# Optimization experiments

Hardware: AMD Instinct MI355X
Metric: run time of the kernel (lower is better)

The kernel has to match this reference:

```python
import jax, jax.numpy as jnp
import numpy as np

FT = 0.2  # clip floor (init arg ft)

def _norm_mat(m):
    # matrix / (count of nonzeros along last dim + 1e-30)
    deg = jnp.sum(m != 0, axis=-1, keepdims=True).astype(m.dtype)
    return m / (deg + 1e-30)

def _l2n(x):
    return x / (jnp.linalg.norm(x, axis=-1, keepdims=True) + 1e-30)

def setup_inputs():
    B, L, D, H, O = 2, 2048, 64, 64, 128
    N = 2 * L
    ks = jax.random.split(jax.random.key(0), 30)
    u = lambda i, s: jax.random.uniform(ks[i], s, jnp.float32)
    g = lambda i, s: jax.random.normal(ks[i], s, jnp.float32) * 0.05
    inp = {}
    inp['word_outputs_0'] = g(0, (B, L, D))
    inp['word_outputs_1'] = g(1, (B, L, D))
    inp['node_hidden'] = g(2, (B, D))
    inp['op_embedding'] = g(3, (B, O, D))
    inp['word_exist_sequence'] = (u(4, (B, N)) < 0.8).astype(jnp.float32)
    inp['word_exist_matrix'] = (u(5, (B, N, N)) < 0.8).astype(jnp.float32)
    inp['word_operator'] = (u(6, (B, N, O)) < 0.02).astype(jnp.float32)
    inp['word_word'] = (u(7, (B, N, N)) < 0.01).astype(jnp.float32)
    inp['depend_0'] = (u(8, (B, L, L)) < 0.05).astype(jnp.float32)
    inp['depend_1'] = (u(9, (B, L, L)) < 0.05).astype(jnp.float32)
    inp['goal_word'] = u(10, (B, N))
    names = [('Wg', (D, H)), ('bg', (H,)), ('Wwk', (D, H)), ('bwk', (H,)),
             ('Wws', (D, H)), ('bws', (H,)), ('Wo', (D, D)), ('bo', (D,)),
             ('Wupd', (3 * H, D)), ('bupd', (D,)), ('Wf', (3 * H + D, D)), ('bf', (D,)),
             ('Wf2', (2 * D, D)), ('bf2', (D,)), ('Wout', (D, D)), ('bout', (D,))]
    for i, (nm, s) in enumerate(names):
        inp[nm] = g(11 + i, s)
    return inp

def _forward(w0, w1, nh, opE, wes, wem, wop, ww, d0, d1, gw,
             Wg, bg, Wwk, bwk, Wws, bws, Wo, bo, Wupd, bupd, Wf, bf, Wf2, bf2, Wout, bout):
    all_w = jnp.concatenate([w0, w1], axis=1)                      # [B,N,D]
    goal_trans = (nh @ Wg + bg)[:, None, :]                        # [B,1,H] (broadcast = expand)
    word_g = _l2n(goal_trans * gw[..., None])                      # [B,N,H]
    word_w_k = _l2n(jnp.matmul(_norm_mat(ww * wem), all_w @ Wwk + bwk))
    ws0 = jnp.matmul(_norm_mat(d0), w0 @ Wws + bws)
    ws1 = jnp.matmul(_norm_mat(d1), w1 @ Wws + bws)
    word_w_s = _l2n(jnp.concatenate([ws0, ws1], axis=1))           # [B,N,H]
    neigh = jnp.concatenate([word_g, word_w_k, word_w_s], axis=-1)  # [B,N,3H]
    forget = jax.nn.sigmoid(jnp.concatenate([all_w, word_g, word_w_k, word_w_s], axis=-1) @ Wf + bf)
    word_updated = jnp.maximum(forget, FT) * all_w + (1.0 - forget) * jax.nn.relu(neigh @ Wupd + bupd)
    adj_op = _norm_mat(jnp.swapaxes(wes[..., None] * wop, 1, 2))   # [B,O,N]
    word_op = jnp.matmul(adj_op, word_updated @ Wo + bo)           # [B,O,D]
    forget2 = jax.nn.sigmoid(jnp.concatenate([opE, word_op], axis=-1) @ Wf2 + bf2)
    op_out = jnp.maximum(forget2, FT) * opE + (1.0 - forget2) * jax.nn.relu(word_op @ Wout + bout)
    # original returns (split(word_updated), op_embedding); concat along node axis here
    return jnp.concatenate([word_updated, op_out], axis=1)         # [B,N+O,D]

def reference(word_outputs_0, word_outputs_1, node_hidden, op_embedding,
              word_exist_sequence, word_exist_matrix, word_operator, word_word,
              depend_0, depend_1, goal_word,
              Wg, bg, Wwk, bwk, Wws, bws, Wo, bo, Wupd, bupd, Wf, bf, Wf2, bf2, Wout, bout):
    return _forward(word_outputs_0, word_outputs_1, node_hidden, op_embedding,
                    word_exist_sequence, word_exist_matrix, word_operator, word_word,
                    depend_0, depend_1, goal_word,
                    Wg, bg, Wwk, bwk, Wws, bws, Wo, bo, Wupd, bupd, Wf, bf, Wf2, bf2, Wout, bout)
```

## Files before the change

### kernel.cpp

```cpp
#include <hip/hip_runtime.h>
#include <cstdint>

typedef unsigned short u16;
typedef unsigned long long u64;

__device__ __forceinline__ u16 f2b(float f){
  union { float f; uint32_t i; } v; v.f = f;
  uint32_t r = v.i + 0x7FFFu + ((v.i >> 16) & 1u);
  return (u16)(r >> 16);
}
__device__ __forceinline__ float b2f(u16 u){
  union { uint32_t i; float f; } v; v.i = ((uint32_t)u) << 16; return v.f;
}
__device__ __forceinline__ float sigmoidf(float x){ return 1.0f / (1.0f + __expf(-x)); }

__device__ __forceinline__ void gl_lds4(const void* g, void* l){
  __builtin_amdgcn_global_load_lds((const __attribute__((address_space(1))) void*)g,
                                   (__attribute__((address_space(3))) void*)l, 4, 0, 0);
}
#define WAIT_VM0() __builtin_amdgcn_s_waitcnt(0x0F70)

__global__ __launch_bounds__(256) void k_bits_all(
    const float* __restrict__ ww, const float* __restrict__ wem,
    const float* __restrict__ d0, const float* __restrict__ d1,
    const float* __restrict__ wes, const float* __restrict__ wop,
    const float* __restrict__ w0, const float* __restrict__ w1,
    const float* __restrict__ nh, const float* __restrict__ Wg, const float* __restrict__ bg,
    const float* __restrict__ Wf, const float* __restrict__ Wupd, const float* __restrict__ Wo,
    u16* __restrict__ psumB, int* __restrict__ pcntB,
    u16* __restrict__ psumD, int* __restrict__ pcntD,
    u64* __restrict__ bitOp, float* __restrict__ ghat,
    uint32_t* __restrict__ pkWf, uint32_t* __restrict__ pkWu, uint32_t* __restrict__ pkWo){
  __shared__ int q[4][256];
  __shared__ float rows[4][16][64];
  int tid = threadIdx.x;
  if (blockIdx.x >= 12544){
    int aux = blockIdx.x - 12544;
    if (aux == 16){
      if (tid < 128){
        int b = tid >> 6, h = tid & 63;
        float g = bg[h];
        for (int d = 0; d < 64; ++d) g += nh[b*64 + d] * Wg[d*64 + h];
        float ss = g * g;
        #pragma unroll
        for (int o = 32; o > 0; o >>= 1) ss += __shfl_xor(ss, o, 64);
        ghat[b*64 + h] = g / (sqrtf(ss) + 1e-30f);
      }
      return;
    }
    for (int k = tid; k < 1024; k += 256){
      int i = aux*1024 + k;
      const float* src; uint32_t* dst; int li;
      if (i < 8192){ src = Wf; dst = pkWf; li = i; }
      else if (i < 14336){ src = Wupd; dst = pkWu; li = i - 8192; }
      else { src = Wo; dst = pkWo; li = i - 14336; }
      int k2 = li >> 6, ln = li & 63;
      dst[li] = (uint32_t)f2b(src[(2*k2)*64 + ln]) | ((uint32_t)f2b(src[(2*k2+1)*64 + ln]) << 16);
    }
    return;
  }
  int wave = tid >> 6, lane = tid & 63;
  int wid = blockIdx.x*4 + wave;
  if (wid >= 49152){
    int ng0 = (wid - 49152) * 8;
    #pragma unroll
    for (int i = 0; i < 8; ++i){
      int n = ng0 + i;
      float vx = wop[(size_t)n*128 + lane];
      float vy = wop[(size_t)n*128 + 64 + lane];
      float e  = wes[n];
      u64 m0 = __ballot((e != 0.f) && (vx != 0.f));
      u64 m1 = __ballot((e != 0.f) && (vy != 0.f));
      if (lane == 0) bitOp[(size_t)n*2]     = m0;
      if (lane == 1) bitOp[(size_t)n*2 + 1] = m1;
    }
    return;
  }
  const float *A, *B;
  const float *srcA, *srcB;
  int jbase, thresh;
  u16* ps; int* pc;
  if (wid < 32768){
    int row = wid >> 2, chunk = wid & 3;
    int b = row >> 12;
    A = ww  + (size_t)row*4096 + chunk*1024;
    B = wem + (size_t)row*4096 + chunk*1024;
    srcA = w0 + (size_t)b*131072 + lane;
    srcB = w1 + (size_t)b*131072 - 131072 + lane;
    jbase = chunk*1024; thresh = 2048;
    ps = psumB + (size_t)wid*64; pc = pcntB + wid;
  } else {
    int idx = wid - 32768;
    int rowp = idx >> 1, chunk = idx & 1;
    if (rowp < 4096){
      int b = rowp >> 11;
      A = d0 + (size_t)rowp*2048 + chunk*1024;
      srcA = w0 + (size_t)b*131072 + lane;
    } else {
      int rr = rowp - 4096, b = rr >> 11;
      A = d1 + (size_t)rr*2048 + chunk*1024;
      srcA = w1 + (size_t)b*131072 + lane;
    }
    B = A; srcB = srcA;
    jbase = chunk*1024; thresh = 4096;
    ps = psumD + (size_t)idx*64; pc = pcntD + idx;
  }
  const float4* ap = (const float4*)A + lane;
  const float4* bp = (const float4*)B + lane;
  float4 a0 = ap[0], a1 = ap[64], a2 = ap[128], a3 = ap[192];
  float4 b0 = bp[0], b1 = bp[64], b2 = bp[128], b3 = bp[192];
  u64 myw = 0;
#define B4(i, va, vb) { \
  u64 m0 = __ballot((va.x != 0.f) && (vb.x != 0.f)); \
  u64 m1 = __ballot((va.y != 0.f) && (vb.y != 0.f)); \
  u64 m2 = __ballot((va.z != 0.f) && (vb.z != 0.f)); \
  u64 m3 = __ballot((va.w != 0.f) && (vb.w != 0.f)); \
  if (lane == (i)*4 + 0) myw = m0; \
  if (lane == (i)*4 + 1) myw = m1; \
  if (lane == (i)*4 + 2) myw = m2; \
  if (lane == (i)*4 + 3) myw = m3; }
  B4(0, a0, b0) B4(1, a1, b1) B4(2, a2, b2) B4(3, a3, b3)
#undef B4
  int c = __popcll(myw);
  int pre = c;
  #pragma unroll
  for (int off = 1; off < 64; off <<= 1){
    int t = __shfl_up(pre, off, 64);
    if (lane >= off) pre += t;
  }
  int total = __shfl(pre, 63, 64);
  int base = pre - c;
  int colhi = (lane >> 2) * 256 + (lane & 3);
  u64 m = myw;
  while (m){
    int p = __builtin_ctzll(m); m &= m - 1;
    q[wave][base++] = colhi + p*4;
  }
#define GPJ(qv) (((jbase + (qv)) < thresh ? srcA : srcB) + (size_t)(jbase + (qv))*64)
  float acc = 0.f;
  int i = 0;
  for (; i + 16 <= total; i += 16){
    int4 c0 = *(const int4*)&q[wave][i];
    int4 c1 = *(const int4*)&q[wave][i + 4];
    int4 c2 = *(const int4*)&q[wave][i + 8];
    int4 c3 = *(const int4*)&q[wave][i + 12];
    gl_lds4(GPJ(c0.x), &rows[wave][ 0][0]);
    gl_lds4(GPJ(c0.y), &rows[wave][ 1][0]);
    gl_lds4(GPJ(c0.z), &rows[wave][ 2][0]);
    gl_lds4(GPJ(c0.w), &rows[wave][ 3][0]);
    gl_lds4(GPJ(c1.x), &rows[wave][ 4][0]);
    gl_lds4(GPJ(c1.y), &rows[wave][ 5][0]);
    gl_lds4(GPJ(c1.z), &rows[wave][ 6][0]);
    gl_lds4(GPJ(c1.w), &rows[wave][ 7][0]);
    gl_lds4(GPJ(c2.x), &rows[wave][ 8][0]);
    gl_lds4(GPJ(c2.y), &rows[wave][ 9][0]);
    gl_lds4(GPJ(c2.z), &rows[wave][10][0]);
    gl_lds4(GPJ(c2.w), &rows[wave][11][0]);
    gl_lds4(GPJ(c3.x), &rows[wave][12][0]);
    gl_lds4(GPJ(c3.y), &rows[wave][13][0]);
    gl_lds4(GPJ(c3.z), &rows[wave][14][0]);
    gl_lds4(GPJ(c3.w), &rows[wave][15][0]);
    WAIT_VM0();
    float s0 = 0.f, s1 = 0.f, s2 = 0.f, s3 = 0.f;
    #pragma unroll
    for (int r = 0; r < 4; ++r){
      s0 += rows[wave][r][lane];
      s1 += rows[wave][4 + r][lane];
      s2 += rows[wave][8 + r][lane];
      s3 += rows[wave][12 + r][lane];
    }
    acc += (s0 + s1) + (s2 + s3);
  }
  for (; i < total; ++i) acc += *GPJ(q[wave][i]);
#undef GPJ
  ps[lane] = f2b(acc);
  if (lane == 0) pc[0] = total;
}

__global__ __launch_bounds__(256) void k_fin(
    const u16* __restrict__ psumB, const int* __restrict__ pcntB,
    const u16* __restrict__ psumD, const int* __restrict__ pcntD,
    const float* __restrict__ Wwk, const float* __restrict__ bwk,
    const float* __restrict__ Wws, const float* __restrict__ bws,
    u16* __restrict__ wwkn, u16* __restrict__ wwsn){
  __shared__ float sWk[4096], sWs[4096];
  int tid = threadIdx.x, lane = tid & 63, wave = tid >> 6;
  for (int i = tid; i < 1024; i += 256){
    ((float4*)sWk)[i] = ((const float4*)Wwk)[i];
    ((float4*)sWs)[i] = ((const float4*)Wws)[i];
  }
  __syncthreads();
  int wid = blockIdx.x*4 + wave;
  float S; float y; const float* sW; u16* outp; size_t oidx;
  if (wid < 8192){
    S = b2f(psumB[((size_t)wid*4 + 0)*64 + lane]) + b2f(psumB[((size_t)wid*4 + 1)*64 + lane])
      + b2f(psumB[((size_t)wid*4 + 2)*64 + lane]) + b2f(psumB[((size_t)wid*4 + 3)*64 + lane]);
    int T = pcntB[wid*4] + pcntB[wid*4 + 1] + pcntB[wid*4 + 2] + pcntB[wid*4 + 3];
    y = (float)T * bwk[lane]; sW = sWk; outp = wwkn; oidx = wid;
  } else {
    int rp = wid - 8192;
    S = b2f(psumD[((size_t)rp*2 + 0)*64 + lane]) + b2f(psumD[((size_t)rp*2 + 1)*64 + lane]);
    int T = pcntD[rp*2] + pcntD[rp*2 + 1];
    y = (float)T * bws[lane]; sW = sWs; outp = wwsn;
    int b, n;
    if (rp < 4096){ b = rp >> 11; n = rp & 2047; }
    else { int rr = rp - 4096; b = rr >> 11; n = 2048 + (rr & 2047); }
    oidx = (size_t)b*4096 + n;
  }
  #pragma unroll 8
  for (int d = 0; d < 64; ++d) y += __shfl(S, d, 64) * sW[d*64 + lane];
  float ss = y * y;
  #pragma unroll
  for (int o = 32; o > 0; o >>= 1) ss += __shfl_xor(ss, o, 64);
  outp[oidx*64 + lane] = f2b(y / (sqrtf(ss) + 1e-30f));
}

__global__ __launch_bounds__(256, 2) void k_update(
    const float* __restrict__ w0, const float* __restrict__ w1,
    const float* __restrict__ gw, const float* __restrict__ ghat,
    const u16* __restrict__ wwkn, const u16* __restrict__ wwsn,
    const uint32_t* __restrict__ pkWf, const uint32_t* __restrict__ pkWu,
    const uint32_t* __restrict__ pkWo,
    const float* __restrict__ bf, const float* __restrict__ bupd, const float* __restrict__ bo,
    float* __restrict__ out, float* __restrict__ WUo){
  __shared__ uint32_t pWf[8192];
  __shared__ uint32_t pWu[6144];
  __shared__ uint32_t pWo[2048];
  __shared__ float xsh[4][256];
  int tid = threadIdx.x;
  for (int i = tid; i < 2048; i += 256) ((uint4*)pWf)[i] = ((const uint4*)pkWf)[i];
  for (int i = tid; i < 1536; i += 256) ((uint4*)pWu)[i] = ((const uint4*)pkWu)[i];
  for (int i = tid; i < 512;  i += 256) ((uint4*)pWo)[i] = ((const uint4*)pkWo)[i];
  __syncthreads();
  int lane = tid & 63, wave = tid >> 6;
  float bff = bf[lane], bup = bupd[lane], boo = bo[lane];
  float aw[4], wgv[4], wk[4], wsv[4];
  #pragma unroll
  for (int t = 0; t < 4; ++t){
    int row = blockIdx.x*4 + wave + t*2048;
    int b = row >> 12, n = row & 4095;
    aw[t] = (n < 2048) ? w0[((size_t)(b*2048 + n))*64 + lane]
                       : w1[((size_t)(b*2048 + n - 2048))*64 + lane];
    float gvv = gw[b*4096 + n];
    wgv[t] = (gvv != 0.f) ? ghat[b*64 + lane] : 0.f;
    wk[t]  = b2f(wwkn[(size_t)row*64 + lane]);
    wsv[t] = b2f(wwsn[(size_t)row*64 + lane]);
  }
  #pragma unroll
  for (int t = 0; t < 4; ++t){
    int row = blockIdx.x*4 + wave + t*2048;
    int b = row >> 12, n = row & 4095;
    xsh[wave][lane] = aw[t]; xsh[wave][64 + lane] = wgv[t];
    xsh[wave][128 + lane] = wk[t]; xsh[wave][192 + lane] = wsv[t];
    float f = bff, u = bup;
    #pragma unroll 8
    for (int k2 = 0; k2 < 32; ++k2){
      float2 xv = *(const float2*)&xsh[wave][2*k2];
      uint32_t wf = pWf[k2*64 + lane];
      f += xv.x * b2f((u16)wf) + xv.y * b2f((u16)(wf >> 16));
    }
    #pragma unroll 8
    for (int k2 = 32; k2 < 128; ++k2){
      float2 xv = *(const float2*)&xsh[wave][2*k2];
      uint32_t wf = pWf[k2*64 + lane];
      uint32_t wu = pWu[(k2 - 32)*64 + lane];
      f += xv.x * b2f((u16)wf) + xv.y * b2f((u16)(wf >> 16));
      u += xv.x * b2f((u16)wu) + xv.y * b2f((u16)(wu >> 16));
    }
    f = sigmoidf(f);
    u = fmaxf(u, 0.f);
    float wu = fmaxf(f, 0.2f) * aw[t] + (1.f - f) * u;
    out[((size_t)b*4224 + n)*64 + lane] = wu;
    float o = boo;
    #pragma unroll 8
    for (int k2 = 0; k2 < 32; ++k2){
      uint32_t wo2 = pWo[k2*64 + lane];
      o += __shfl(wu, 2*k2, 64) * b2f((u16)wo2) + __shfl(wu, 2*k2 + 1, 64) * b2f((u16)(wo2 >> 16));
    }
    WUo[(size_t)row*64 + lane] = o;
  }
}

__global__ __launch_bounds__(256) void k_opfin(
    const u64* __restrict__ bitOp, const float* __restrict__ WUo,
    const float* __restrict__ opE,
    const float* __restrict__ Wf2, const float* __restrict__ bf2,
    const float* __restrict__ Wout, const float* __restrict__ bout,
    float* __restrict__ out){
  __shared__ float sW2[8192];
  __shared__ float sWo[4096];
  __shared__ int q[4][96];
  __shared__ float sacc[4][64];
  __shared__ int scnt[4];
  __shared__ float xsh[128];
  int tid = threadIdx.x, lane = tid & 63, wave = tid >> 6;
  for (int i = tid; i < 2048; i += 256) ((float4*)sW2)[i] = ((const float4*)Wf2)[i];
  for (int i = tid; i < 1024; i += 256) ((float4*)sWo)[i] = ((const float4*)Wout)[i];
  int rowIdx = blockIdx.x;
  int b = rowIdx >> 7, o = rowIdx & 127;
  int wrd = o >> 6, bit = o & 63;
  const u64* bp = bitOp + (size_t)b*8192 + (size_t)wave*2048 + wrd;
  u64 lt = (1ULL << lane) - 1ULL;
  u64 vv[16];
  #pragma unroll
  for (int it = 0; it < 16; ++it) vv[it] = bp[(size_t)(it*64 + lane)*2];
  int cnt = 0;
  #pragma unroll
  for (int it = 0; it < 16; ++it){
    bool nz = (vv[it] >> bit) & 1ULL;
    u64 m = __ballot(nz);
    if (nz) q[wave][cnt + (int)__popcll(m & lt)] = wave*1024 + it*64 + lane;
    cnt += (int)__popcll(m);
  }
  const float* Xb = WUo + (size_t)b*4096*64 + lane;
  float acc = 0.f;
  int i = 0;
  for (; i + 8 <= cnt; i += 8){
    int4 c0 = *(const int4*)&q[wave][i];
    int4 c1 = *(const int4*)&q[wave][i + 4];
    float v0 = Xb[(size_t)c0.x*64], v1 = Xb[(size_t)c0.y*64];
    float v2 = Xb[(size_t)c0.z*64], v3 = Xb[(size_t)c0.w*64];
    float v4 = Xb[(size_t)c1.x*64], v5 = Xb[(size_t)c1.y*64];
    float v6 = Xb[(size_t)c1.z*64], v7 = Xb[(size_t)c1.w*64];
    acc += ((v0 + v1) + (v2 + v3)) + ((v4 + v5) + (v6 + v7));
  }
  for (; i < cnt; ++i) acc += Xb[(size_t)q[wave][i]*64];
  sacc[wave][lane] = acc;
  if (lane == 0) scnt[wave] = cnt;
  __syncthreads();
  if (wave == 0){
    float t = sacc[0][lane] + sacc[1][lane] + sacc[2][lane] + sacc[3][lane];
    float deg = (float)(scnt[0] + scnt[1] + scnt[2] + scnt[3]);
    float wo = t / (deg + 1e-30f);
    float e  = opE[(size_t)rowIdx*64 + lane];
    xsh[lane] = e; xsh[64 + lane] = wo;
    float f = bf2[lane], u = bout[lane];
    #pragma unroll 8
    for (int k = 0; k < 128; ++k) f += xsh[k] * sW2[k*64 + lane];
    #pragma unroll 8
    for (int d = 0; d < 64; ++d)  u += xsh[64 + d] * sWo[d*64 + lane];
    f = sigmoidf(f);
    u = fmaxf(u, 0.f);
    float res = fmaxf(f, 0.2f) * e + (1.f - f) * u;
    out[((size_t)b*4224 + 4096 + o)*64 + lane] = res;
  }
}

extern "C" void kernel_launch(void* const* d_in, const int* in_sizes, int n_in,
                              void* d_out, int out_size, void* d_ws, size_t ws_size,
                              hipStream_t stream){
  const float* w0   = (const float*)d_in[0];
  const float* w1   = (const float*)d_in[1];
  const float* nh   = (const float*)d_in[2];
  const float* opE  = (const float*)d_in[3];
  const float* wes  = (const float*)d_in[4];
  const float* wem  = (const float*)d_in[5];
  const float* wop  = (const float*)d_in[6];
  const float* ww   = (const float*)d_in[7];
  const float* d0   = (const float*)d_in[8];
  const float* d1   = (const float*)d_in[9];
  const float* gw   = (const float*)d_in[10];
  const float* Wg   = (const float*)d_in[11];
  const float* bg   = (const float*)d_in[12];
  const float* Wwk  = (const float*)d_in[13];
  const float* bwk  = (const float*)d_in[14];
  const float* Wws  = (const float*)d_in[15];
  const float* bws  = (const float*)d_in[16];
  const float* Wo   = (const float*)d_in[17];
  const float* bo   = (const float*)d_in[18];
  const float* Wupd = (const float*)d_in[19];
  const float* bupd = (const float*)d_in[20];
  const float* Wf   = (const float*)d_in[21];
  const float* bf   = (const float*)d_in[22];
  const float* Wf2  = (const float*)d_in[23];
  const float* bf2  = (const float*)d_in[24];
  const float* Wout = (const float*)d_in[25];
  const float* bout = (const float*)d_in[26];

  float* ws    = (float*)d_ws;
  float* ghat  = ws;
  uint32_t* pkWf = (uint32_t*)(ws + 128);
  uint32_t* pkWu = (uint32_t*)(ws + 8320);
  uint32_t* pkWo = (uint32_t*)(ws + 14464);
  u64*  bitOp  = (u64*)(ws + 16512);
  u16*  psumB  = (u16*)(ws + 49280);
  int*  pcntB  = (int*)(ws + 1097856);
  u16*  psumD  = (u16*)(ws + 1130624);
  int*  pcntD  = (int*)(ws + 1654912);
  u16*  wwkn   = (u16*)(ws + 1671296);
  u16*  wwsn   = (u16*)(ws + 1933440);
  float* WUo   = ws + 2195584;
  float* out   = (float*)d_out;

  k_bits_all<<<12561, 256, 0, stream>>>(ww, wem, d0, d1, wes, wop, w0, w1,
                                        nh, Wg, bg, Wf, Wupd, Wo,
                                        psumB, pcntB, psumD, pcntD,
                                        bitOp, ghat, pkWf, pkWu, pkWo);
  k_fin<<<4096, 256, 0, stream>>>(psumB, pcntB, psumD, pcntD,
                                  Wwk, bwk, Wws, bws, wwkn, wwsn);
  k_update<<<512, 256, 0, stream>>>(w0, w1, gw, ghat, wwkn, wwsn,
                                    pkWf, pkWu, pkWo, bf, bupd, bo, out, WUo);
  k_opfin<<<256, 256, 0, stream>>>(bitOp, WUo, opE, Wf2, bf2, Wout, bout, out);
}
```

Measured before the change: 443.4 us.

## Replace sparse gather aggregation with dense bf16 MFMA over mask tiles

Replaces the ballot/compact/gather sparse aggregation of word rows with a dense matrix multiply on MFMA. The 0/1 mask is packed as bf16, and the features are pre-transposed into hi/lo bf16 pairs so that products keep near-fp32 accuracy. Neighbor counts come from an extra MFMA against a ones vector. This trades irregular gathers and LDS staging for streaming dense reads and matrix-core compute, at the cost of doing dense FLOPs on very sparse masks plus a new transpose kernel. k_fin is also reshaped so each block handles four rows, cutting its grid to a quarter.

Measured after the change: 492.2 us. +11.0%, slower.

```diff
diff --git a/kernel.cpp b/kernel.cpp
--- a/kernel.cpp
+++ b/kernel.cpp
@@ -3,6 +3,8 @@
 
 typedef unsigned short u16;
 typedef unsigned long long u64;
+typedef __attribute__((ext_vector_type(8))) short bf16x8;
+typedef __attribute__((ext_vector_type(4))) float f32x4;
 
 __device__ __forceinline__ u16 f2b(float f){
   union { float f; uint32_t i; } v; v.f = f;
@@ -14,55 +16,78 @@
 }
 __device__ __forceinline__ float sigmoidf(float x){ return 1.0f / (1.0f + __expf(-x)); }
 
-__device__ __forceinline__ void gl_lds4(const void* g, void* l){
-  __builtin_amdgcn_global_load_lds((const __attribute__((address_space(1))) void*)g,
-                                   (__attribute__((address_space(3))) void*)l, 4, 0, 0);
-}
-#define WAIT_VM0() __builtin_amdgcn_s_waitcnt(0x0F70)
-
-__global__ __launch_bounds__(256) void k_bits_all(
+#define MFMA16(a,b,c) __builtin_amdgcn_mfma_f32_16x16x32_bf16(a,b,c,0,0,0)
+
+__global__ __launch_bounds__(256) void k_prep(
+    const float* __restrict__ w0, const float* __restrict__ w1,
+    u16* __restrict__ wThi, u16* __restrict__ wTlo){
+  __shared__ float tile[64][65];
+  int tid = threadIdx.x;
+  int t = blockIdx.x;
+  int b = t >> 6, kt = t & 63;
+  int k0 = kt * 64;
+  const float* src = (k0 < 2048) ? (w0 + ((size_t)b*2048 + k0)*64)
+                                 : (w1 + ((size_t)b*2048 + (k0 - 2048))*64);
+  int r0 = tid >> 6, c = tid & 63;
+  #pragma unroll
+  for (int it = 0; it < 16; ++it){
+    int n = it*4 + r0;
+    tile[n][c] = src[(size_t)n*64 + c];
+  }
+  __syncthreads();
+  #pragma unroll
+  for (int it = 0; it < 16; ++it){
+    int d = it*4 + r0;
+    float v = tile[c][d];
+    u16 h = f2b(v);
+    float lo = v - b2f(h);
+    size_t o = ((size_t)b*64 + d)*4096 + k0 + c;
+    wThi[o] = h;
+    wTlo[o] = f2b(lo);
+  }
+}
+
+__global__ __launch_bounds__(256) void k_mask(
     const float* __restrict__ ww, const float* __restrict__ wem,
     const float* __restrict__ d0, const float* __restrict__ d1,
     const float* __restrict__ wes, const float* __restrict__ wop,
-    const float* __restrict__ w0, const float* __restrict__ w1,
+    const u16* __restrict__ wThi, const u16* __restrict__ wTlo,
     const float* __restrict__ nh, const float* __restrict__ Wg, const float* __restrict__ bg,
     const float* __restrict__ Wf, const float* __restrict__ Wupd, const float* __restrict__ Wo,
     u16* __restrict__ psumB, int* __restrict__ pcntB,
     u16* __restrict__ psumD, int* __restrict__ pcntD,
     u64* __restrict__ bitOp, float* __restrict__ ghat,
     uint32_t* __restrict__ pkWf, uint32_t* __restrict__ pkWu, uint32_t* __restrict__ pkWo){
-  __shared__ int q[4][256];
-  __shared__ float rows[4][16][64];
-  int tid = threadIdx.x;
-  if (blockIdx.x >= 12544){
-    int aux = blockIdx.x - 12544;
-    if (aux == 16){
-      if (tid < 128){
-        int b = tid >> 6, h = tid & 63;
-        float g = bg[h];
-        for (int d = 0; d < 64; ++d) g += nh[b*64 + d] * Wg[d*64 + h];
-        float ss = g * g;
-        #pragma unroll
-        for (int o = 32; o > 0; o >>= 1) ss += __shfl_xor(ss, o, 64);
-        ghat[b*64 + h] = g / (sqrtf(ss) + 1e-30f);
+  int tid = threadIdx.x, wave = tid >> 6, lane = tid & 63;
+  int bid = blockIdx.x;
+  if (bid >= 768){
+    if (bid >= 1024){
+      int aux = bid - 1024;
+      if (aux == 16){
+        if (tid < 128){
+          int b = tid >> 6, h = tid & 63;
+          float g = bg[h];
+          for (int d = 0; d < 64; ++d) g += nh[b*64 + d] * Wg[d*64 + h];
+          float ss = g * g;
+          #pragma unroll
+          for (int o = 32; o > 0; o >>= 1) ss += __shfl_xor(ss, o, 64);
+          ghat[b*64 + h] = g / (sqrtf(ss) + 1e-30f);
+        }
+        return;
+      }
+      for (int k = tid; k < 1024; k += 256){
+        int i = aux*1024 + k;
+        const float* src; uint32_t* dst; int li;
+        if (i < 8192){ src = Wf; dst = pkWf; li = i; }
+        else if (i < 14336){ src = Wupd; dst = pkWu; li = i - 8192; }
+        else { src = Wo; dst = pkWo; li = i - 14336; }
+        int k2 = li >> 6, ln = li & 63;
+        dst[li] = (uint32_t)f2b(src[(2*k2)*64 + ln]) | ((uint32_t)f2b(src[(2*k2+1)*64 + ln]) << 16);
       }
       return;
     }
-    for (int k = tid; k < 1024; k += 256){
-      int i = aux*1024 + k;
-      const float* src; uint32_t* dst; int li;
-      if (i < 8192){ src = Wf; dst = pkWf; li = i; }
-      else if (i < 14336){ src = Wupd; dst = pkWu; li = i - 8192; }
-      else { src = Wo; dst = pkWo; li = i - 14336; }
-      int k2 = li >> 6, ln = li & 63;
-      dst[li] = (uint32_t)f2b(src[(2*k2)*64 + ln]) | ((uint32_t)f2b(src[(2*k2+1)*64 + ln]) << 16);
-    }
-    return;
-  }
-  int wave = tid >> 6, lane = tid & 63;
-  int wid = blockIdx.x*4 + wave;
-  if (wid >= 49152){
-    int ng0 = (wid - 49152) * 8;
+    int w = (bid - 768)*4 + wave;
+    int ng0 = w * 8;
     #pragma unroll
     for (int i = 0; i < 8; ++i){
       int n = ng0 + i;
@@ -76,105 +101,107 @@
     }
     return;
   }
-  const float *A, *B;
-  const float *srcA, *srcB;
-  int jbase, thresh;
-  u16* ps; int* pc;
-  if (wid < 32768){
-    int row = wid >> 2, chunk = wid & 3;
-    int b = row >> 12;
-    A = ww  + (size_t)row*4096 + chunk*1024;
-    B = wem + (size_t)row*4096 + chunk*1024;
-    srcA = w0 + (size_t)b*131072 + lane;
-    srcB = w1 + (size_t)b*131072 - 131072 + lane;
-    jbase = chunk*1024; thresh = 2048;
-    ps = psumB + (size_t)wid*64; pc = pcntB + wid;
+  bool big; int wb, kOffW, tBase, tStride;
+  const float *mArow, *mBrow; size_t ldm;
+  u16* psArr; int* pcArr;
+  if (bid < 512){
+    int rowblk = bid >> 2, kq = bid & 3;
+    int bb = rowblk >> 6;
+    int grow = bb*4096 + (rowblk & 63)*64 + wave*16;
+    mArow = ww  + (size_t)grow*4096 + kq*1024;
+    mBrow = wem + (size_t)grow*4096 + kq*1024;
+    ldm = 4096; big = true;
+    wb = bb; kOffW = kq*1024;
+    tBase = grow*4 + kq; tStride = 4;
+    psArr = psumB; pcArr = pcntB;
   } else {
-    int idx = wid - 32768;
-    int rowp = idx >> 1, chunk = idx & 1;
-    if (rowp < 4096){
-      int b = rowp >> 11;
-      A = d0 + (size_t)rowp*2048 + chunk*1024;
-      srcA = w0 + (size_t)b*131072 + lane;
-    } else {
-      int rr = rowp - 4096, b = rr >> 11;
-      A = d1 + (size_t)rr*2048 + chunk*1024;
-      srcA = w1 + (size_t)b*131072 + lane;
-    }
-    B = A; srcB = srcA;
-    jbase = chunk*1024; thresh = 4096;
-    ps = psumD + (size_t)idx*64; pc = pcntD + idx;
-  }
-  const float4* ap = (const float4*)A + lane;
-  const float4* bp = (const float4*)B + lane;
-  float4 a0 = ap[0], a1 = ap[64], a2 = ap[128], a3 = ap[192];
-  float4 b0 = bp[0], b1 = bp[64], b2 = bp[128], b3 = bp[192];
-  u64 myw = 0;
-#define B4(i, va, vb) { \
-  u64 m0 = __ballot((va.x != 0.f) && (vb.x != 0.f)); \
-  u64 m1 = __ballot((va.y != 0.f) && (vb.y != 0.f)); \
-  u64 m2 = __ballot((va.z != 0.f) && (vb.z != 0.f)); \
-  u64 m3 = __ballot((va.w != 0.f) && (vb.w != 0.f)); \
-  if (lane == (i)*4 + 0) myw = m0; \
-  if (lane == (i)*4 + 1) myw = m1; \
-  if (lane == (i)*4 + 2) myw = m2; \
-  if (lane == (i)*4 + 3) myw = m3; }
-  B4(0, a0, b0) B4(1, a1, b1) B4(2, a2, b2) B4(3, a3, b3)
-#undef B4
-  int c = __popcll(myw);
-  int pre = c;
-  #pragma unroll
-  for (int off = 1; off < 64; off <<= 1){
-    int t = __shfl_up(pre, off, 64);
-    if (lane >= off) pre += t;
-  }
-  int total = __shfl(pre, 63, 64);
-  int base = pre - c;
-  int colhi = (lane >> 2) * 256 + (lane & 3);
-  u64 m = myw;
-  while (m){
-    int p = __builtin_ctzll(m); m &= m - 1;
-    q[wave][base++] = colhi + p*4;
-  }
-#define GPJ(qv) (((jbase + (qv)) < thresh ? srcA : srcB) + (size_t)(jbase + (qv))*64)
-  float acc = 0.f;
-  int i = 0;
-  for (; i + 16 <= total; i += 16){
-    int4 c0 = *(const int4*)&q[wave][i];
-    int4 c1 = *(const int4*)&q[wave][i + 4];
-    int4 c2 = *(const int4*)&q[wave][i + 8];
-    int4 c3 = *(const int4*)&q[wave][i + 12];
-    gl_lds4(GPJ(c0.x), &rows[wave][ 0][0]);
-    gl_lds4(GPJ(c0.y), &rows[wave][ 1][0]);
-    gl_lds4(GPJ(c0.z), &rows[wave][ 2][0]);
-    gl_lds4(GPJ(c0.w), &rows[wave][ 3][0]);
-    gl_lds4(GPJ(c1.x), &rows[wave][ 4][0]);
-    gl_lds4(GPJ(c1.y), &rows[wave][ 5][0]);
-    gl_lds4(GPJ(c1.z), &rows[wave][ 6][0]);
-    gl_lds4(GPJ(c1.w), &rows[wave][ 7][0]);
-    gl_lds4(GPJ(c2.x), &rows[wave][ 8][0]);
-    gl_lds4(GPJ(c2.y), &rows[wave][ 9][0]);
-    gl_lds4(GPJ(c2.z), &rows[wave][10][0]);
-    gl_lds4(GPJ(c2.w), &rows[wave][11][0]);
-    gl_lds4(GPJ(c3.x), &rows[wave][12][0]);
-    gl_lds4(GPJ(c3.y), &rows[wave][13][0]);
-    gl_lds4(GPJ(c3.z), &rows[wave][14][0]);
-    gl_lds4(GPJ(c3.w), &rows[wave][15][0]);
-    WAIT_VM0();
-    float s0 = 0.f, s1 = 0.f, s2 = 0.f, s3 = 0.f;
-    #pragma unroll
-    for (int r = 0; r < 4; ++r){
-      s0 += rows[wave][r][lane];
-      s1 += rows[wave][4 + r][lane];
-      s2 += rows[wave][8 + r][lane];
-      s3 += rows[wave][12 + r][lane];
-    }
-    acc += (s0 + s1) + (s2 + s3);
-  }
-  for (; i < total; ++i) acc += *GPJ(q[wave][i]);
-#undef GPJ
-  ps[lane] = f2b(acc);
-  if (lane == 0) pc[0] = total;
+    int i = bid - 512;
+    int inst = i >> 6, r6 = i & 63;
+    int rowblkL = r6 >> 1, kh = r6 & 1;
+    int prow = inst*2048 + rowblkL*64 + wave*16;
+    const float* marr = (inst < 2) ? d0 : d1;
+    int mrow = (inst < 2) ? prow : (prow - 4096);
+    mArow = marr + (size_t)mrow*2048 + kh*1024;
+    mBrow = mArow; ldm = 2048; big = false;
+    wb = inst & 1; kOffW = ((inst >= 2) ? 2048 : 0) + kh*1024;
+    tBase = prow*2 + kh; tStride = 2;
+    psArr = psumD; pcArr = pcntD;
+  }
+  int col = lane & 15, oct = lane >> 4;
+  const float* pa = mArow + (size_t)col*ldm + oct*8;
+  const float* pc = mBrow + (size_t)col*ldm + oct*8;
+  const u16* ph = wThi + ((size_t)wb*64 + col)*4096 + kOffW + oct*8;
+  const u16* pl = wTlo + ((size_t)wb*64 + col)*4096 + kOffW + oct*8;
+
+  f32x4 acc0 = {0.f,0.f,0.f,0.f}, acc1 = acc0, acc2 = acc0, acc3 = acc0, accD = acc0;
+  union { uint32_t w[4]; bf16x8 v; } onesU;
+  onesU.w[0] = onesU.w[1] = onesU.w[2] = onesU.w[3] = 0x3F803F80u;
+  bf16x8 ones = onesU.v;
+
+  float4 a0 = *(const float4*)pa;
+  float4 a1 = *(const float4*)(pa + 4);
+  float4 c0v = {0,0,0,0}, c1v = {0,0,0,0};
+  if (big){ c0v = *(const float4*)pc; c1v = *(const float4*)(pc + 4); }
+  bf16x8 h0 = *(const bf16x8*)ph;
+  bf16x8 h1 = *(const bf16x8*)(ph + 65536);
+  bf16x8 h2 = *(const bf16x8*)(ph + 131072);
+  bf16x8 h3 = *(const bf16x8*)(ph + 196608);
+  bf16x8 l0 = *(const bf16x8*)pl;
+  bf16x8 l1 = *(const bf16x8*)(pl + 65536);
+  bf16x8 l2 = *(const bf16x8*)(pl + 131072);
+  bf16x8 l3 = *(const bf16x8*)(pl + 196608);
+
+  #pragma unroll 1
+  for (int s = 0; s < 32; ++s){
+    float4 wa0 = a0, wa1 = a1, wc0 = c0v, wc1 = c1v;
+    bf16x8 bh0 = h0, bh1 = h1, bh2 = h2, bh3 = h3;
+    bf16x8 bl0 = l0, bl1 = l1, bl2 = l2, bl3 = l3;
+    if (s < 31){
+      const float* qa = pa + (size_t)(s+1)*32;
+      a0 = *(const float4*)qa; a1 = *(const float4*)(qa + 4);
+      if (big){
+        const float* qc = pc + (size_t)(s+1)*32;
+        c0v = *(const float4*)qc; c1v = *(const float4*)(qc + 4);
+      }
+      const u16* qh = ph + (size_t)(s+1)*32;
+      h0 = *(const bf16x8*)qh;
+      h1 = *(const bf16x8*)(qh + 65536);
+      h2 = *(const bf16x8*)(qh + 131072);
+      h3 = *(const bf16x8*)(qh + 196608);
+      const u16* ql = pl + (size_t)(s+1)*32;
+      l0 = *(const bf16x8*)ql;
+      l1 = *(const bf16x8*)(ql + 65536);
+      l2 = *(const bf16x8*)(ql + 131072);
+      l3 = *(const bf16x8*)(ql + 196608);
+    }
+#define SEL(x,y) ((x != 0.f) && (!big || (y != 0.f)))
+    union { uint32_t w[4]; bf16x8 v; } af;
+    af.w[0] = (SEL(wa0.x,wc0.x)?0x3F80u:0u) | (SEL(wa0.y,wc0.y)?0x3F800000u:0u);
+    af.w[1] = (SEL(wa0.z,wc0.z)?0x3F80u:0u) | (SEL(wa0.w,wc0.w)?0x3F800000u:0u);
+    af.w[2] = (SEL(wa1.x,wc1.x)?0x3F80u:0u) | (SEL(wa1.y,wc1.y)?0x3F800000u:0u);
+    af.w[3] = (SEL(wa1.z,wc1.z)?0x3F80u:0u) | (SEL(wa1.w,wc1.w)?0x3F800000u:0u);
+#undef SEL
+    bf16x8 a = af.v;
+    acc0 = MFMA16(a, bh0, acc0);
+    acc0 = MFMA16(a, bl0, acc0);
+    acc1 = MFMA16(a, bh1, acc1);
+    acc1 = MFMA16(a, bl1, acc1);
+    acc2 = MFMA16(a, bh2, acc2);
+    acc2 = MFMA16(a, bl2, acc2);
+    acc3 = MFMA16(a, bh3, acc3);
+    acc3 = MFMA16(a, bl3, acc3);
+    accD = MFMA16(a, ones, accD);
+  }
+  #pragma unroll
+  for (int r = 0; r < 4; ++r){
+    size_t t = (size_t)tBase + (size_t)(oct*4 + r) * tStride;
+    u16* prow = psArr + t*64;
+    prow[ 0 + col] = f2b(acc0[r]);
+    prow[16 + col] = f2b(acc1[r]);
+    prow[32 + col] = f2b(acc2[r]);
+    prow[48 + col] = f2b(acc3[r]);
+    if (col == 0) pcArr[t] = (int)(accD[r] + 0.5f);
+  }
 }
 
 __global__ __launch_bounds__(256) void k_fin(
@@ -190,29 +217,31 @@
     ((float4*)sWs)[i] = ((const float4*)Wws)[i];
   }
   __syncthreads();
-  int wid = blockIdx.x*4 + wave;
-  float S; float y; const float* sW; u16* outp; size_t oidx;
-  if (wid < 8192){
-    S = b2f(psumB[((size_t)wid*4 + 0)*64 + lane]) + b2f(psumB[((size_t)wid*4 + 1)*64 + lane])
-      + b2f(psumB[((size_t)wid*4 + 2)*64 + lane]) + b2f(psumB[((size_t)wid*4 + 3)*64 + lane]);
-    int T = pcntB[wid*4] + pcntB[wid*4 + 1] + pcntB[wid*4 + 2] + pcntB[wid*4 + 3];
-    y = (float)T * bwk[lane]; sW = sWk; outp = wwkn; oidx = wid;
-  } else {
-    int rp = wid - 8192;
-    S = b2f(psumD[((size_t)rp*2 + 0)*64 + lane]) + b2f(psumD[((size_t)rp*2 + 1)*64 + lane]);
-    int T = pcntD[rp*2] + pcntD[rp*2 + 1];
-    y = (float)T * bws[lane]; sW = sWs; outp = wwsn;
-    int b, n;
-    if (rp < 4096){ b = rp >> 11; n = rp & 2047; }
-    else { int rr = rp - 4096; b = rr >> 11; n = 2048 + (rr & 2047); }
-    oidx = (size_t)b*4096 + n;
-  }
-  #pragma unroll 8
-  for (int d = 0; d < 64; ++d) y += __shfl(S, d, 64) * sW[d*64 + lane];
-  float ss = y * y;
-  #pragma unroll
-  for (int o = 32; o > 0; o >>= 1) ss += __shfl_xor(ss, o, 64);
-  outp[oidx*64 + lane] = f2b(y / (sqrtf(ss) + 1e-30f));
+  for (int r = 0; r < 4; ++r){
+    int wid = blockIdx.x*4 + wave + r*4096;
+    float S; float y; const float* sW; u16* outp; size_t oidx;
+    if (wid < 8192){
+      S = b2f(psumB[((size_t)wid*4 + 0)*64 + lane]) + b2f(psumB[((size_t)wid*4 + 1)*64 + lane])
+        + b2f(psumB[((size_t)wid*4 + 2)*64 + lane]) + b2f(psumB[((size_t)wid*4 + 3)*64 + lane]);
+      int T = pcntB[wid*4] + pcntB[wid*4 + 1] + pcntB[wid*4 + 2] + pcntB[wid*4 + 3];
+      y = (float)T * bwk[lane]; sW = sWk; outp = wwkn; oidx = wid;
+    } else {
+      int rp = wid - 8192;
+      S = b2f(psumD[((size_t)rp*2 + 0)*64 + lane]) + b2f(psumD[((size_t)rp*2 + 1)*64 + lane]);
+      int T = pcntD[rp*2] + pcntD[rp*2 + 1];
+      y = (float)T * bws[lane]; sW = sWs; outp = wwsn;
+      int b, n;
+      if (rp < 4096){ b = rp >> 11; n = rp & 2047; }
+      else { int rr = rp - 4096; b = rr >> 11; n = 2048 + (rr & 2047); }
+      oidx = (size_t)b*4096 + n;
+    }
+    #pragma unroll 8
+    for (int d = 0; d < 64; ++d) y += __shfl(S, d, 64) * sW[d*64 + lane];
+    float ss = y * y;
+    #pragma unroll
+    for (int o = 32; o > 0; o >>= 1) ss += __shfl_xor(ss, o, 64);
+    outp[oidx*64 + lane] = f2b(y / (sqrtf(ss) + 1e-30f));
+  }
 }
 
 __global__ __launch_bounds__(256, 2) void k_update(
@@ -390,13 +419,16 @@
   u16*  wwkn   = (u16*)(ws + 1671296);
   u16*  wwsn   = (u16*)(ws + 1933440);
   float* WUo   = ws + 2195584;
+  u16*  wThi   = (u16*)(ws + 2719872);
+  u16*  wTlo   = (u16*)(ws + 2982016);
   float* out   = (float*)d_out;
 
-  k_bits_all<<<12561, 256, 0, stream>>>(ww, wem, d0, d1, wes, wop, w0, w1,
-                                        nh, Wg, bg, Wf, Wupd, Wo,
-                                        psumB, pcntB, psumD, pcntD,
-                                        bitOp, ghat, pkWf, pkWu, pkWo);
-  k_fin<<<4096, 256, 0, stream>>>(psumB, pcntB, psumD, pcntD,
+  k_prep<<<128, 256, 0, stream>>>(w0, w1, wThi, wTlo);
+  k_mask<<<1041, 256, 0, stream>>>(ww, wem, d0, d1, wes, wop, wThi, wTlo,
+                                   nh, Wg, bg, Wf, Wupd, Wo,
+                                   psumB, pcntB, psumD, pcntD,
+                                   bitOp, ghat, pkWf, pkWu, pkWo);
+  k_fin<<<1024, 256, 0, stream>>>(psumB, pcntB, psumD, pcntD,
                                   Wwk, bwk, Wws, bws, wwkn, wwsn);
   k_update<<<512, 256, 0, stream>>>(w0, w1, gw, ghat, wwkn, wwsn,
                                     pkWf, pkWu, pkWo, bf, bupd, bo, out, WUo);
```
